# Optimization experiments

Hardware: AMD Instinct MI355X
Metric: run time of the kernel (lower is better)

The kernel has to match this reference:

```python
import jax, jax.numpy as jnp
import numpy as np
from jax import lax

K = 7          # local attention kernel size
DIL = 2        # dilation
PAD = 6        # padding -> same spatial size
BN_EPS = 1e-5


def setup_inputs() -> dict:
    key = jax.random.key(0)
    ks = jax.random.split(key, 4)
    B, C, H, W = 16, 256, 56, 56
    x = jax.random.normal(ks[0], (B, C, H, W), dtype=jnp.float32)
    # conv weights scaled for stable activations
    w1 = jax.random.normal(ks[1], (128, C, K, K), dtype=jnp.float32) * 0.02
    b1 = jnp.zeros((128,), dtype=jnp.float32)
    w2 = jax.random.normal(ks[2], (49, 128, 1, 1), dtype=jnp.float32) * 0.05
    b2 = jnp.zeros((49,), dtype=jnp.float32)
    gamma = jnp.ones((49,), dtype=jnp.float32)
    beta = jnp.zeros((49,), dtype=jnp.float32)
    running_mean = jnp.zeros((49,), dtype=jnp.float32)
    running_var = jnp.ones((49,), dtype=jnp.float32)
    return {"x": x, "w1": w1, "b1": b1, "w2": w2, "b2": b2,
            "gamma": gamma, "beta": beta,
            "running_mean": running_mean, "running_var": running_var}


def _picanet_l(x, w1, b1, w2, b2, gamma, beta, running_mean, running_var):
    B, C, H, W = x.shape
    # conv1: 7x7, dilation 2, padding 6 (same size)
    k = lax.conv_general_dilated(
        x, w1, window_strides=(1, 1), padding=((PAD, PAD), (PAD, PAD)),
        rhs_dilation=(DIL, DIL),
        dimension_numbers=("NCHW", "OIHW", "NCHW"))
    k = jax.nn.relu(k + b1[None, :, None, None])
    # conv2: 1x1 -> 49 channels
    k = jnp.einsum("bchw,oc->bohw", k, w2[:, :, 0, 0]) + b2[None, :, None, None]
    # BatchNorm (eval-style, running stats), then relu + softmax over the 49 taps
    inv = gamma * lax.rsqrt(running_var + BN_EPS)
    k = (k - running_mean[None, :, None, None]) * inv[None, :, None, None] + beta[None, :, None, None]
    k = jax.nn.relu(k)
    attn = jax.nn.softmax(k, axis=1)  # [B, 49, H, W]
    # unfold-gather + weighted sum, expressed as 49 shifted slices of the
    # zero-padded input (matches F.unfold(x, 7, dilation=2, padding=6)).
    xpad = jnp.pad(x, ((0, 0), (0, 0), (PAD, PAD), (PAD, PAD)))
    out = jnp.zeros_like(x)
    for i in range(K):
        for j in range(K):
            tap = xpad[:, :, DIL * i: DIL * i + H, DIL * j: DIL * j + W]  # [B,C,H,W]
            out = out + tap * attn[:, i * K + j][:, None]
    return out


def reference(x, w1, b1, w2, b2, gamma, beta, running_mean, running_var):
    return _picanet_l(x, w1, b1, w2, b2, gamma, beta, running_mean, running_var)
```

## Files before the change

kernel.cpp:

```cpp
#include <hip/hip_runtime.h>

typedef _Float16 f16;
typedef __attribute__((__ext_vector_type__(2))) _Float16 f16x2;
typedef __attribute__((__ext_vector_type__(4))) _Float16 f16x4;
typedef __attribute__((__ext_vector_type__(8))) _Float16 f16x8;
typedef __attribute__((__ext_vector_type__(4))) float f32x4;

#define GLDS16(g, l) __builtin_amdgcn_global_load_lds( \
    (const __attribute__((address_space(1))) void*)(g), \
    (__attribute__((address_space(3))) void*)(l), 16, 0, 0)


__global__ __launch_bounds__(256) void zero_border(uint4* __restrict__ xp) {
  const int i = blockIdx.x * 256 + threadIdx.x;
  int idx4;
  if (i < 417792) {
    int u = i % 2176;
    int row12 = i / 2176;
    int b = row12 / 12, r12 = row12 % 12;
    int r = (r12 < 6) ? r12 : r12 + 56;
    idx4 = (b * 68 + r) * 2176 + u;
  } else {
    int j = i - 417792;
    int u = j % 192;
    int run = j / 192;
    int side = run & 1;
    int br = run >> 1;
    int r = br % 56 + 6, b = br / 56;
    idx4 = (b * 68 + r) * 2176 + (side ? 62 * 32 : 0) + u;
  }
  xp[idx4] = make_uint4(0u, 0u, 0u, 0u);
}

__global__ __launch_bounds__(256) void transpose_cast(
    const float* __restrict__ x, f16* __restrict__ xpad) {
  __shared__ f16 t16[56][258];
  const int bh = blockIdx.x;
  const int h = bh % 56, b = bh / 56;
  const float* xp = x + (size_t)b * 256 * 3136 + h * 56;
  for (int f = threadIdx.x; f < 256 * 56; f += 256) {
    int c = f / 56, w = f % 56;
    t16[w][c] = (f16)xp[(size_t)c * 3136 + w];
  }
  __syncthreads();
  f16* op = xpad + (((size_t)(b * 68) + h + 6) * 68 + 6) * 256;
  for (int g = threadIdx.x; g < 56 * 32; g += 256) {
    int w = g >> 5, c0 = (g & 31) * 8;
    *(f16x8*)(op + (size_t)w * 256 + c0) = *(const f16x8*)&t16[w][c0];
  }
}

__global__ __launch_bounds__(256) void w1_transform(
    const float* __restrict__ w1, f16* __restrict__ w1h) {
  const int idx = blockIdx.x * 256 + threadIdx.x;
  const int co = idx >> 8, c = idx & 255;
  const int half = c >> 7, cc = (c >> 5) & 3, q = (c >> 3) & 3, e = c & 7;
  const int f = co >> 4, l15 = co & 15;
  const size_t base =
      ((((size_t)(half * 4 + cc) * 8 + f) * 64 + q * 16 + l15) * 8 + e);
  const float* src = w1 + ((size_t)co * 256 + c) * 49;
#pragma unroll 7
  for (int ij = 0; ij < 49; ++ij)
    w1h[base + (size_t)ij * 32768] = (f16)src[ij];
}

__global__ __launch_bounds__(256, 2) void conv1_gemm(
    const f16* __restrict__ xpad, const f16* __restrict__ w1h,
    f16* __restrict__ kbuf) {
  __shared__ f16 strip[16 * 68 * 32];

  const int tid = threadIdx.x;
  const int wid = tid >> 6, lane = tid & 63;
  const int pphys = blockIdx.x;
  const int bid = (pphys & 7) * 56 + (pphys >> 3);
  const int half = bid & 1;
  const int sid = bid >> 1;
  const int b = sid / 14;
  const int h0 = (sid % 14) * 4;

  const int l15 = lane & 15;
  const int q = lane >> 4;
  const int qb = (l15 >> 1) & 3;

  const int mbase = (wid >> 1) * 7;
  const int nbase = (wid & 1) * 4;

  int arow_off[7];
#pragma unroll
  for (int mm = 0; mm < 7; ++mm) {
    int p = (mbase + mm) * 16 + l15;
    int rw = p / 56;
    int w = p - 56 * rw;
    arow_off[mm] = (rw * 68 + w) * 64;
  }

  const char* xg = (const char*)xpad +
                   ((size_t)(b * 68 + h0)) * (68 * 512) + half * 256;
  const char* wB = (const char*)w1h;
  char* Ss = (char*)strip;

  const int half4 = half * 4;
  auto loadB = [&](int cc, int ij, int nn) -> f16x8 {
    int off = (((ij * 8 + half4 + cc) * 8 + nbase + nn) * 64 + lane) * 16;
    return *(const f16x8*)(wB + off);
  };
  auto baseOff = [&](int ij) -> int {
    const int i = (int)((unsigned)ij / 7u);
    const int j = ij - 7 * i;
    return i * 8704 + j * 128 + ((q ^ ((qb + j) & 3)) << 4);
  };

  f32x4 acc[7][4] = {};
  f16x8 pb0 = loadB(0, 0, 0), pb1 = loadB(0, 0, 1);
  f16x8 pb2 = loadB(0, 0, 2), pb3 = loadB(0, 0, 3);
  f16x8 A0[7], A1[7];

  for (int cc = 0; cc < 4; ++cc) {
    const int chb = cc * 64;
    __syncthreads();
#pragma unroll
    for (int rr = 0; rr < 17; ++rr) {
      int s = rr * 256 + tid;
      int r = (int)((unsigned)s / 272u);
      int rem = s - r * 272;
      int col = rem >> 2, q4 = rem & 3;
      int qq = q4 ^ ((col >> 1) & 3);
      GLDS16(xg + (size_t)r * (68 * 512) + col * 512 + chb + qq * 16,
             Ss + (rr * 256 + wid * 64) * 16);
    }
    __syncthreads();

    {
      const int bo = baseOff(0);
#pragma unroll
      for (int mm = 0; mm < 7; ++mm)
        A0[mm] = *(const f16x8*)(Ss + arow_off[mm] + bo);
    }

    auto tapStep = [&](f16x8* Acur, f16x8* Anxt, int ij, bool loadA) {
      f16x8 b0 = pb0, b1 = pb1, b2 = pb2, b3 = pb3;
      int nij = ij + 1, ncc = cc;
      if (nij == 49) { nij = 0; ++ncc; }
      if (ncc < 4) {
        pb0 = loadB(ncc, nij, 0);
        pb1 = loadB(ncc, nij, 1);
        pb2 = loadB(ncc, nij, 2);
        pb3 = loadB(ncc, nij, 3);
      }
      if (loadA) {
        const int bo = baseOff(ij + 1);
#pragma unroll
        for (int mm = 0; mm < 7; ++mm)
          Anxt[mm] = *(const f16x8*)(Ss + arow_off[mm] + bo);
      }
#pragma unroll
      for (int mm = 0; mm < 7; ++mm) {
        acc[mm][0] = __builtin_amdgcn_mfma_f32_16x16x32_f16(Acur[mm], b0,
                                                            acc[mm][0], 0, 0, 0);
        acc[mm][1] = __builtin_amdgcn_mfma_f32_16x16x32_f16(Acur[mm], b1,
                                                            acc[mm][1], 0, 0, 0);
        acc[mm][2] = __builtin_amdgcn_mfma_f32_16x16x32_f16(Acur[mm], b2,
                                                            acc[mm][2], 0, 0, 0);
        acc[mm][3] = __builtin_amdgcn_mfma_f32_16x16x32_f16(Acur[mm], b3,
                                                            acc[mm][3], 0, 0, 0);
      }
    };

    for (int pt = 0; pt < 24; ++pt) {
      tapStep(A0, A1, 2 * pt, true);
      tapStep(A1, A0, 2 * pt + 1, true);
    }
    tapStep(A0, A1, 48, false);
  }

  f16* kh = kbuf + (size_t)half * (50176 * 128);
  const int pbase = (b * 56 + h0) * 56;
#pragma unroll
  for (int mm = 0; mm < 7; ++mm) {
#pragma unroll
    for (int nn = 0; nn < 4; ++nn) {
      const int co = (nbase + nn) * 16 + l15;
#pragma unroll
      for (int r = 0; r < 4; ++r) {
        int p = (mbase + mm) * 16 + q * 4 + r;
        int rw = p / 56;
        int w = p - 56 * rw;
        kh[(size_t)(pbase + rw * 56 + w) * 128 + co] = (f16)acc[mm][nn][r];
      }
    }
  }
}

__global__ __launch_bounds__(128) void conv2_bn_softmax(
    const f16* __restrict__ kbuf, const float* __restrict__ b1,
    const float* __restrict__ w2, const float* __restrict__ b2,
    const float* __restrict__ gamma, const float* __restrict__ beta,
    const float* __restrict__ rmean, const float* __restrict__ rvar,
    float* __restrict__ attn) {
  __shared__ f16 w2s[49 * 128];
  __shared__ float b1s[128];
  __shared__ float outs[128 * 49];
  for (int i = threadIdx.x; i < 49 * 128; i += 128) w2s[i] = (f16)w2[i];
  if (threadIdx.x < 128) b1s[threadIdx.x] = b1[threadIdx.x];
  __syncthreads();
  const int p = blockIdx.x * 128 + threadIdx.x;
  float acc[49];
#pragma unroll
  for (int o = 0; o < 49; ++o) acc[o] = 0.f;
  const f16x8* ka = (const f16x8*)(kbuf + (size_t)p * 128);
  const f16x8* kb = (const f16x8*)(kbuf + (size_t)50176 * 128 + (size_t)p * 128);
  for (int u = 0; u < 16; ++u) {
    f16x8 va = ka[u], vb = kb[u];
    f16x2 kvh[4];
#pragma unroll
    for (int j = 0; j < 4; ++j) {
      float s0 = (float)va[2 * j] + (float)vb[2 * j] + b1s[u * 8 + 2 * j];
      float s1 =
          (float)va[2 * j + 1] + (float)vb[2 * j + 1] + b1s[u * 8 + 2 * j + 1];
      s0 = s0 > 0.f ? s0 : 0.f;
      s1 = s1 > 0.f ? s1 : 0.f;
      kvh[j] = f16x2{(f16)s0, (f16)s1};
    }
#pragma unroll
    for (int o = 0; o < 49; ++o) {
      f16x8 wv = *(const f16x8*)(w2s + o * 128 + u * 8);
#if __has_builtin(__builtin_amdgcn_fdot2)
      acc[o] = __builtin_amdgcn_fdot2(kvh[0], f16x2{wv[0], wv[1]}, acc[o], false);
      acc[o] = __builtin_amdgcn_fdot2(kvh[1], f16x2{wv[2], wv[3]}, acc[o], false);
      acc[o] = __builtin_amdgcn_fdot2(kvh[2], f16x2{wv[4], wv[5]}, acc[o], false);
      acc[o] = __builtin_amdgcn_fdot2(kvh[3], f16x2{wv[6], wv[7]}, acc[o], false);
#else
#pragma unroll
      for (int j = 0; j < 4; ++j)
        acc[o] += (float)kvh[j][0] * (float)wv[2 * j] +
                  (float)kvh[j][1] * (float)wv[2 * j + 1];
#endif
    }
  }
  float mx = -1e30f;
#pragma unroll
  for (int o = 0; o < 49; ++o) {
    float s = acc[o] + b2[o];
    float inv = gamma[o] * rsqrtf(rvar[o] + 1e-5f);
    s = (s - rmean[o]) * inv + beta[o];
    s = s > 0.f ? s : 0.f;
    acc[o] = s;
    mx = fmaxf(mx, s);
  }
  float sum = 0.f;
#pragma unroll
  for (int o = 0; o < 49; ++o) {
    float e = __expf(acc[o] - mx);
    acc[o] = e;
    sum += e;
  }
  const float rinv = 1.f / sum;
  float* orow = outs + threadIdx.x * 49;
#pragma unroll
  for (int o = 0; o < 49; ++o) orow[o] = acc[o] * rinv;
  __syncthreads();
  float* ab = attn + (size_t)blockIdx.x * (128 * 49);
  for (int i = threadIdx.x; i < 128 * 49; i += 128) ab[i] = outs[i];
}

__global__ __launch_bounds__(896, 1) void aggregate2(
    const f16* __restrict__ xpad, const float* __restrict__ attn,
    float* __restrict__ out) {
  __shared__ float t[256][57];
  const int pp = blockIdx.x;
  const int bh = (pp & 7) * 112 + (pp >> 3);
  const int h = bh % 56, b = bh / 56;
  const int tid = threadIdx.x;
  const int wid = tid >> 6, lane = tid & 63;
  const int q = (wid < 7) ? wid * 8 : (wid - 7) * 8 + 1;

  int ap[4];
#pragma unroll
  for (int p = 0; p < 4; ++p) ap[p] = ((b * 56 + h) * 56 + q + 2 * p) * 49;

  float acc[4][4] = {};
  const f16* rowb = xpad + ((size_t)(b * 68 + h) * 68 + q) * 256 + 4 * lane;

  for (int i = 0; i < 7; ++i) {
    const f16* rb = rowb + (size_t)(2 * i * 68) * 256;
#pragma unroll
    for (int tt = 0; tt < 10; ++tt) {
      f16x4 xv = *(const f16x4*)(rb + tt * 512);
      float xf[4];
#pragma unroll
      for (int k = 0; k < 4; ++k) xf[k] = (float)xv[k];
#pragma unroll
      for (int p = 0; p < 4; ++p) {
        const int j = tt - p;
        if (j >= 0 && j < 7) {
          const float a = attn[ap[p] + i * 7 + j];
#pragma unroll
          for (int k = 0; k < 4; ++k) acc[p][k] = fmaf(a, xf[k], acc[p][k]);
        }
      }
    }
  }

#pragma unroll
  for (int p = 0; p < 4; ++p)
#pragma unroll
    for (int k = 0; k < 4; ++k) t[4 * lane + k][q + 2 * p] = acc[p][k];
  __syncthreads();
  float* ob = out + ((size_t)b * 256 * 56 + h) * 56;
  for (int f = tid; f < 256 * 56; f += 896) {
    int c = f / 56, w = f % 56;
    ob[(size_t)c * 3136 + w] = t[c][w];
  }
}

extern "C" void kernel_launch(void* const* d_in, const int* in_sizes, int n_in,
                              void* d_out, int out_size, void* d_ws,
                              size_t ws_size, hipStream_t stream) {
  const float* x = (const float*)d_in[0];
  const float* w1 = (const float*)d_in[1];
  const float* b1 = (const float*)d_in[2];
  const float* w2 = (const float*)d_in[3];
  const float* b2 = (const float*)d_in[4];
  const float* gamma = (const float*)d_in[5];
  const float* beta = (const float*)d_in[6];
  const float* rmean = (const float*)d_in[7];
  const float* rvar = (const float*)d_in[8];
  float* out = (float*)d_out;

  char* ws = (char*)d_ws;
  f16* xpad = (f16*)ws;
  f16* w1h = (f16*)(ws + 37879808);
  f16* kbuf = (f16*)(ws + 41091072);
  float* attn = (float*)(ws + 66781184);

  hipLaunchKernelGGL(zero_border, dim3(2976), dim3(256), 0, stream,
                     (uint4*)xpad);
  hipLaunchKernelGGL(transpose_cast, dim3(896), dim3(256), 0, stream, x, xpad);
  hipLaunchKernelGGL(w1_transform, dim3(128), dim3(256), 0, stream, w1, w1h);
  hipLaunchKernelGGL(conv1_gemm, dim3(448), dim3(256), 0, stream, xpad, w1h,
                     kbuf);
  hipLaunchKernelGGL(conv2_bn_softmax, dim3(392), dim3(128), 0, stream, kbuf,
                     b1, w2, b2, gamma, beta, rmean, rvar, attn);
  hipLaunchKernelGGL(aggregate2, dim3(896), dim3(896), 0, stream, xpad, attn,
                     out);
}
```

Baseline: 247.0 us.

## Drop split-K halves in conv1 GEMM and double-buffer LDS channel strips

conv1_gemm no longer splits the input channels across two blocks with partial kbuf outputs. Each block now loops over all 8 channel chunks and ping-pongs between two LDS strips, so the next chunk's async global->LDS load overlaps the current chunk's MFMAs. This removes the second partial-sum buffer and the add in conv2. The cost is half the grid (224 blocks, fewer than the CU count on MI355X), double the LDS per block, and launch bounds lowered to one block per SM, so occupancy and parallelism drop.

```diff
diff --git a/kernel.cpp b/kernel.cpp
--- a/kernel.cpp
+++ b/kernel.cpp
@@ -54,27 +54,25 @@
     const float* __restrict__ w1, f16* __restrict__ w1h) {
   const int idx = blockIdx.x * 256 + threadIdx.x;
   const int co = idx >> 8, c = idx & 255;
-  const int half = c >> 7, cc = (c >> 5) & 3, q = (c >> 3) & 3, e = c & 7;
+  const int cc8 = c >> 5, q = (c >> 3) & 3, e = c & 7;
   const int f = co >> 4, l15 = co & 15;
-  const size_t base =
-      ((((size_t)(half * 4 + cc) * 8 + f) * 64 + q * 16 + l15) * 8 + e);
+  const size_t base = ((((size_t)cc8 * 8 + f) * 64 + q * 16 + l15) * 8 + e);
   const float* src = w1 + ((size_t)co * 256 + c) * 49;
 #pragma unroll 7
   for (int ij = 0; ij < 49; ++ij)
     w1h[base + (size_t)ij * 32768] = (f16)src[ij];
 }
 
-__global__ __launch_bounds__(256, 2) void conv1_gemm(
+__global__ __launch_bounds__(256, 1) void conv1_gemm(
     const f16* __restrict__ xpad, const f16* __restrict__ w1h,
     f16* __restrict__ kbuf) {
-  __shared__ f16 strip[16 * 68 * 32];
+  __shared__ f16 strip0[16 * 68 * 32];
+  __shared__ f16 strip1[16 * 68 * 32];
 
   const int tid = threadIdx.x;
   const int wid = tid >> 6, lane = tid & 63;
   const int pphys = blockIdx.x;
-  const int bid = (pphys & 7) * 56 + (pphys >> 3);
-  const int half = bid & 1;
-  const int sid = bid >> 1;
+  const int sid = (pphys & 7) * 28 + (pphys >> 3);
   const int b = sid / 14;
   const int h0 = (sid % 14) * 4;
 
@@ -94,14 +92,13 @@
     arow_off[mm] = (rw * 68 + w) * 64;
   }
 
-  const char* xg = (const char*)xpad +
-                   ((size_t)(b * 68 + h0)) * (68 * 512) + half * 256;
+  const char* xg = (const char*)xpad + ((size_t)(b * 68 + h0)) * (68 * 512);
   const char* wB = (const char*)w1h;
-  char* Ss = (char*)strip;
-
-  const int half4 = half * 4;
-  auto loadB = [&](int cc, int ij, int nn) -> f16x8 {
-    int off = (((ij * 8 + half4 + cc) * 8 + nbase + nn) * 64 + lane) * 16;
+  char* Ss0 = (char*)strip0;
+  char* Ss1 = (char*)strip1;
+
+  auto loadB = [&](int cc8, int ij, int nn) -> f16x8 {
+    int off = (((ij * 8 + cc8) * 8 + nbase + nn) * 64 + lane) * 16;
     return *(const f16x8*)(wB + off);
   };
   auto baseOff = [&](int ij) -> int {
@@ -109,15 +106,8 @@
     const int j = ij - 7 * i;
     return i * 8704 + j * 128 + ((q ^ ((qb + j) & 3)) << 4);
   };
-
-  f32x4 acc[7][4] = {};
-  f16x8 pb0 = loadB(0, 0, 0), pb1 = loadB(0, 0, 1);
-  f16x8 pb2 = loadB(0, 0, 2), pb3 = loadB(0, 0, 3);
-  f16x8 A0[7], A1[7];
-
-  for (int cc = 0; cc < 4; ++cc) {
-    const int chb = cc * 64;
-    __syncthreads();
+  auto stage = [&](char* dst, int cc8) {
+    const int chb = cc8 * 64;
 #pragma unroll
     for (int rr = 0; rr < 17; ++rr) {
       int s = rr * 256 + tid;
@@ -126,22 +116,35 @@
       int col = rem >> 2, q4 = rem & 3;
       int qq = q4 ^ ((col >> 1) & 3);
       GLDS16(xg + (size_t)r * (68 * 512) + col * 512 + chb + qq * 16,
-             Ss + (rr * 256 + wid * 64) * 16);
-    }
-    __syncthreads();
+             dst + (rr * 256 + wid * 64) * 16);
+    }
+  };
+
+  f32x4 acc[7][4] = {};
+  f16x8 pb0 = loadB(0, 0, 0), pb1 = loadB(0, 0, 1);
+  f16x8 pb2 = loadB(0, 0, 2), pb3 = loadB(0, 0, 3);
+  f16x8 A0[7], A1[7];
+
+  stage(Ss0, 0);
+  __syncthreads();
+
+  for (int cc8 = 0; cc8 < 8; ++cc8) {
+    char* Sc = (cc8 & 1) ? Ss1 : Ss0;
+    char* Sn = (cc8 & 1) ? Ss0 : Ss1;
+    if (cc8 < 7) stage(Sn, cc8 + 1);
 
     {
       const int bo = baseOff(0);
 #pragma unroll
       for (int mm = 0; mm < 7; ++mm)
-        A0[mm] = *(const f16x8*)(Ss + arow_off[mm] + bo);
+        A0[mm] = *(const f16x8*)(Sc + arow_off[mm] + bo);
     }
 
     auto tapStep = [&](f16x8* Acur, f16x8* Anxt, int ij, bool loadA) {
       f16x8 b0 = pb0, b1 = pb1, b2 = pb2, b3 = pb3;
-      int nij = ij + 1, ncc = cc;
+      int nij = ij + 1, ncc = cc8;
       if (nij == 49) { nij = 0; ++ncc; }
-      if (ncc < 4) {
+      if (ncc < 8) {
         pb0 = loadB(ncc, nij, 0);
         pb1 = loadB(ncc, nij, 1);
         pb2 = loadB(ncc, nij, 2);
@@ -151,7 +154,7 @@
         const int bo = baseOff(ij + 1);
 #pragma unroll
         for (int mm = 0; mm < 7; ++mm)
-          Anxt[mm] = *(const f16x8*)(Ss + arow_off[mm] + bo);
+          Anxt[mm] = *(const f16x8*)(Sc + arow_off[mm] + bo);
       }
 #pragma unroll
       for (int mm = 0; mm < 7; ++mm) {
@@ -171,9 +174,10 @@
       tapStep(A1, A0, 2 * pt + 1, true);
     }
     tapStep(A0, A1, 48, false);
-  }
-
-  f16* kh = kbuf + (size_t)half * (50176 * 128);
+
+    __syncthreads();
+  }
+
   const int pbase = (b * 56 + h0) * 56;
 #pragma unroll
   for (int mm = 0; mm < 7; ++mm) {
@@ -185,7 +189,7 @@
         int p = (mbase + mm) * 16 + q * 4 + r;
         int rw = p / 56;
         int w = p - 56 * rw;
-        kh[(size_t)(pbase + rw * 56 + w) * 128 + co] = (f16)acc[mm][nn][r];
+        kbuf[(size_t)(pbase + rw * 56 + w) * 128 + co] = (f16)acc[mm][nn][r];
       }
     }
   }
@@ -208,15 +212,13 @@
 #pragma unroll
   for (int o = 0; o < 49; ++o) acc[o] = 0.f;
   const f16x8* ka = (const f16x8*)(kbuf + (size_t)p * 128);
-  const f16x8* kb = (const f16x8*)(kbuf + (size_t)50176 * 128 + (size_t)p * 128);
   for (int u = 0; u < 16; ++u) {
-    f16x8 va = ka[u], vb = kb[u];
+    f16x8 va = ka[u];
     f16x2 kvh[4];
 #pragma unroll
     for (int j = 0; j < 4; ++j) {
-      float s0 = (float)va[2 * j] + (float)vb[2 * j] + b1s[u * 8 + 2 * j];
-      float s1 =
-          (float)va[2 * j + 1] + (float)vb[2 * j + 1] + b1s[u * 8 + 2 * j + 1];
+      float s0 = (float)va[2 * j] + b1s[u * 8 + 2 * j];
+      float s1 = (float)va[2 * j + 1] + b1s[u * 8 + 2 * j + 1];
       s0 = s0 > 0.f ? s0 : 0.f;
       s1 = s1 > 0.f ? s1 : 0.f;
       kvh[j] = f16x2{(f16)s0, (f16)s1};
@@ -331,13 +333,13 @@
   f16* xpad = (f16*)ws;
   f16* w1h = (f16*)(ws + 37879808);
   f16* kbuf = (f16*)(ws + 41091072);
-  float* attn = (float*)(ws + 66781184);
+  float* attn = (float*)(ws + 53936128);
 
   hipLaunchKernelGGL(zero_border, dim3(2976), dim3(256), 0, stream,
                      (uint4*)xpad);
   hipLaunchKernelGGL(transpose_cast, dim3(896), dim3(256), 0, stream, x, xpad);
   hipLaunchKernelGGL(w1_transform, dim3(128), dim3(256), 0, stream, w1, w1h);
-  hipLaunchKernelGGL(conv1_gemm, dim3(448), dim3(256), 0, stream, xpad, w1h,
+  hipLaunchKernelGGL(conv1_gemm, dim3(224), dim3(256), 0, stream, xpad, w1h,
                      kbuf);
   hipLaunchKernelGGL(conv2_bn_softmax, dim3(392), dim3(128), 0, stream, kbuf,
                      b1, w2, b2, gamma, beta, rmean, rvar, attn);
```

Result: slower. 294.6 us (+19.3%).
